# Optimization experiments

Measured on AMD Instinct MI355X. Metric: run time of the kernel, lower is better.

Reference implementation:

```python
import jax, jax.numpy as jnp
import numpy as np
import itertools

DIMS = (128, 128, 128)
CHANNELS = 8
BATCH = 2_097_152


def setup_inputs() -> dict:
    key = jax.random.key(0)
    k1, k2 = jax.random.split(key)
    unList = jax.random.uniform(k1, (BATCH, len(DIMS)), dtype=jnp.float32)
    table = jax.random.uniform(k2, DIMS + (CHANNELS,), dtype=jnp.float32)  # initScale=1, initMode='R'
    return {"unList": unList, "table": table}


def reference(unList, table):
    # N-D multilinear (bilinear/trilinear) interpolated table lookup.
    dims = table.shape[:-1]
    n = len(dims)
    c = table.shape[-1]
    dims_f = jnp.asarray(dims, jnp.float32)
    # map normalized coords [0,1] onto grid [0, dim-1]
    scaled = jnp.clip(unList, 0.0, 1.0) * (dims_f - 1.0)          # [B, n]
    i0 = jnp.clip(jnp.floor(scaled), 0.0, dims_f - 2.0).astype(jnp.int32)  # lower corner
    frac = scaled - i0.astype(jnp.float32)                        # [B, n] in [0,1]
    # flatten grid for single-axis gathers
    strides = jnp.asarray([int(np.prod(dims[k + 1:])) for k in range(n)], jnp.int32)
    table_flat = table.reshape(-1, c)                             # [prod(dims), C]
    out = jnp.zeros((unList.shape[0], c), table.dtype)
    # loop over the 2^n corners (8 for 3D) -- small static loop
    for corner in itertools.product((0, 1), repeat=n):
        bits = jnp.asarray(corner, jnp.int32)                     # [n]
        flat_idx = ((i0 + bits) * strides).sum(-1)                # [B]
        w = jnp.prod(jnp.where(jnp.asarray(corner, bool), frac, 1.0 - frac), axis=-1)  # [B]
        out = out + w[:, None] * table_flat[flat_idx]             # gather + weighted sum
    return out
```

## Files before the change

kernel.cpp:

```cpp
#include <hip/hip_runtime.h>


#define DIM 128
#define CH 8
#define NBIN 2048
#define TBYTES 67108864u
#define CHUNK 8192
#define PPT 32
#define SLABB 61440u
#define BPB 4
#define CUR_OFF 8192
#define BASE_OFF 16384
#define REC_OFF 32768

__device__ __forceinline__ int key_of(float ux, float uy) {
    float sx = fminf(fmaxf(ux, 0.0f), 1.0f) * 127.0f;
    float sy = fminf(fmaxf(uy, 0.0f), 1.0f) * 127.0f;
    int x0 = (int)fminf(floorf(sx), 126.0f);
    int y0 = (int)fminf(floorf(sy), 126.0f);
    return (x0 >> 1) * 32 + (y0 >> 2);
}

__global__ __launch_bounds__(256) void k_hist(const float* __restrict__ un,
                                              unsigned* __restrict__ hist, int batch) {
    __shared__ unsigned lh[NBIN];
    for (int i = threadIdx.x; i < NBIN; i += 256) lh[i] = 0;
    __syncthreads();
    int stride = gridDim.x * blockDim.x;
    for (int i = blockIdx.x * blockDim.x + threadIdx.x; i < batch; i += stride)
        atomicAdd(&lh[key_of(un[3 * i], un[3 * i + 1])], 1u);
    __syncthreads();
    for (int i = threadIdx.x; i < NBIN; i += 256)
        if (lh[i]) atomicAdd(&hist[i], lh[i]);
}

__global__ __launch_bounds__(1024) void k_scan(const unsigned* __restrict__ hist,
                                               unsigned* __restrict__ cursor,
                                               unsigned* __restrict__ base) {
    __shared__ unsigned s[1024];
    int t = threadIdx.x;
    unsigned h0 = hist[t * 2], h1 = hist[t * 2 + 1];
    s[t] = h0 + h1;
    __syncthreads();
    for (int off = 1; off < 1024; off <<= 1) {
        unsigned v = (t >= off) ? s[t - off] : 0u;
        __syncthreads();
        s[t] += v;
        __syncthreads();
    }
    unsigned excl = s[t] - (h0 + h1);
    base[t * 2] = excl;           cursor[t * 2] = excl;
    base[t * 2 + 1] = excl + h0;  cursor[t * 2 + 1] = excl + h0;
    if (t == 1023) base[NBIN] = s[1023];
}

__global__ __launch_bounds__(256) void k_scatter(const float* __restrict__ un,
                                                 unsigned* __restrict__ cursor,
                                                 uint2* __restrict__ rec, int batch) {
    __shared__ unsigned lh[NBIN];
    __shared__ unsigned lbase[NBIN];
    int t = threadIdx.x;
    for (int i = t; i < NBIN; i += 256) lh[i] = 0;
    __syncthreads();
    int start = blockIdx.x * CHUNK;
    unsigned kr[PPT];
#pragma unroll
    for (int j = 0; j < PPT; ++j) {
        int i = start + j * 256 + t;
        if (i < batch) {
            int k = key_of(un[3 * i], un[3 * i + 1]);
            unsigned r = atomicAdd(&lh[k], 1u);
            kr[j] = (unsigned)k | (r << 12);
        } else kr[j] = 0u;
    }
    __syncthreads();
    for (int i = t; i < NBIN; i += 256)
        lbase[i] = lh[i] ? atomicAdd(&cursor[i], lh[i]) : 0u;
    __syncthreads();
#pragma unroll
    for (int j = 0; j < PPT; ++j) {
        int i = start + j * 256 + t;
        if (i < batch) {
            unsigned k = kr[j] & 4095u, r = kr[j] >> 12;
            float ux = un[3 * i], uy = un[3 * i + 1], uz = un[3 * i + 2];
            float sx = fminf(fmaxf(ux, 0.0f), 1.0f) * 127.0f;
            float sy = fminf(fmaxf(uy, 0.0f), 1.0f) * 127.0f;
            float sz = fminf(fmaxf(uz, 0.0f), 1.0f) * 127.0f;
            float fx0 = fminf(floorf(sx), 126.0f);
            float fy0 = fminf(floorf(sy), 126.0f);
            float fz0 = fminf(floorf(sz), 126.0f);
            int x0 = (int)fx0, y0 = (int)fy0, z0 = (int)fz0;
            unsigned qx = (unsigned)((sx - fx0) * 2047.0f + 0.5f);
            unsigned qy = (unsigned)((sy - fy0) * 2047.0f + 0.5f);
            unsigned qz = (unsigned)((sz - fz0) * 1023.0f + 0.5f);
            unsigned dx = (unsigned)(x0 & 1);
            unsigned dy = (unsigned)(y0 & 3);
            uint2 rr;
            rr.x = (unsigned)i | (dx << 21) | (dy << 22) | ((unsigned)z0 << 24);
            rr.y = qx | (qy << 11) | (qz << 22);
            rec[lbase[k] + r] = rr;
        }
    }
}

__global__ __launch_bounds__(1024, 4) void k_main(const uint2* __restrict__ rec,
                                                  const float* __restrict__ table,
                                                  const unsigned* __restrict__ base,
                                                  float* __restrict__ out) {
    __shared__ float4 lds4[2 * SLABB / 16];
    char* ldsb = (char*)lds4;
    const char* tb = (const char*)table;

    int b = (int)blockIdx.x;
    int bb = (b & 7) * 64 + (b >> 3);
    int g0 = bb * BPB;

    int t = (int)threadIdx.x;
    int lane = t & 63, wave = t >> 6;
    int p = lane >> 1, h = lane & 1;
    const unsigned hoff = (unsigned)(h << 4);
    const float rs11 = 1.0f / 2047.0f, rs10 = 1.0f / 1023.0f;

#define STAGE(binid, buf) { \
        int X_ = (binid) >> 5, Y_ = (binid) & 31; \
        _Pragma("unroll") \
        for (int k_ = 0; k_ < 4; ++k_) { \
            int c_ = wave + k_ * 16; \
            if (c_ < 60) { \
                int pr_ = c_ >> 2, q4_ = c_ & 3; \
                int p2_ = (pr_ * 13) >> 6; \
                int r2_ = pr_ - p2_ * 5; \
                int gp_ = 2 * X_ + p2_;  if (gp_ > 127) gp_ = 127; \
                int gr_ = 4 * Y_ + r2_;  if (gr_ > 127) gr_ = 127; \
                unsigned go_ = (unsigned)((gp_ * 128 + gr_) * 4096 + q4_ * 1024) \
                             + (unsigned)lane * 16u; \
                __builtin_amdgcn_global_load_lds( \
                    (const __attribute__((address_space(1))) void*)(tb + go_), \
                    (__attribute__((address_space(3))) void*)(ldsb + (buf) * SLABB \
                        + (unsigned)c_ * 1024u), 16, 0, 0); \
            } \
        } }

    STAGE(g0, 0u)

    for (int j = 0; j < BPB; ++j) {
        asm volatile("s_waitcnt vmcnt(0) lgkmcnt(0)" ::: "memory");
        __builtin_amdgcn_s_barrier();
        __builtin_amdgcn_sched_barrier(0);
        if (j + 1 < BPB) STAGE(g0 + j + 1, (unsigned)((j + 1) & 1))
        __builtin_amdgcn_sched_barrier(0);

        unsigned s = base[g0 + j], e = base[g0 + j + 1];
        const char* lb = ldsb + (unsigned)(j & 1) * SLABB;

        for (unsigned idx = s + (unsigned)(wave * 32 + p); idx < e; idx += 512u) {
            uint2 rr = rec[idx];
            unsigned orig = rr.x & 0x1FFFFFu;
            unsigned dx = (rr.x >> 21) & 1u;
            unsigned dy = (rr.x >> 22) & 3u;
            unsigned z0 = (rr.x >> 24) & 0x7Fu;
            float fx = (float)(rr.y & 0x7FFu) * rs11;
            float fy = (float)((rr.y >> 11) & 0x7FFu) * rs11;
            float fz = (float)(rr.y >> 22) * rs10;
            float gxw = 1.0f - fx, gyw = 1.0f - fy, gzw = 1.0f - fz;
            float wA0 = gxw * gyw * gzw, wA1 = gxw * gyw * fz;
            float wB0 = gxw * fy  * gzw, wB1 = gxw * fy  * fz;
            float wC0 = fx  * gyw * gzw, wC1 = fx  * gyw * fz;
            float wD0 = fx  * fy  * gzw, wD1 = fx  * fy  * fz;
            unsigned a = (dx * 5u + dy) * 4096u + z0 * 32u + hoff;
            float4 vA0 = *(const float4*)(lb + a);
            float4 vA1 = *(const float4*)(lb + a + 32u);
            float4 vB0 = *(const float4*)(lb + a + 4096u);
            float4 vB1 = *(const float4*)(lb + a + 4128u);
            float4 vC0 = *(const float4*)(lb + a + 20480u);
            float4 vC1 = *(const float4*)(lb + a + 20512u);
            float4 vD0 = *(const float4*)(lb + a + 24576u);
            float4 vD1 = *(const float4*)(lb + a + 24608u);
            float4 acc;
            acc.x = wA0*vA0.x + wA1*vA1.x + wB0*vB0.x + wB1*vB1.x
                  + wC0*vC0.x + wC1*vC1.x + wD0*vD0.x + wD1*vD1.x;
            acc.y = wA0*vA0.y + wA1*vA1.y + wB0*vB0.y + wB1*vB1.y
                  + wC0*vC0.y + wC1*vC1.y + wD0*vD0.y + wD1*vD1.y;
            acc.z = wA0*vA0.z + wA1*vA1.z + wB0*vB0.z + wB1*vB1.z
                  + wC0*vC0.z + wC1*vC1.z + wD0*vD0.z + wD1*vD1.z;
            acc.w = wA0*vA0.w + wA1*vA1.w + wB0*vB0.w + wB1*vB1.w
                  + wC0*vC0.w + wC1*vC1.w + wD0*vD0.w + wD1*vD1.w;
            *reinterpret_cast<float4*>(out + (size_t)orig * CH + (h << 2)) = acc;
        }
        __builtin_amdgcn_sched_barrier(0);
    }
#undef STAGE
}

__global__ __launch_bounds__(256) void k_naive(const float* __restrict__ un,
                                               const float* __restrict__ table,
                                               float* __restrict__ out, int batch) {
    int b = blockIdx.x * blockDim.x + threadIdx.x;
    if (b >= batch) return;
    float ux = un[3 * b], uy = un[3 * b + 1], uz = un[3 * b + 2];
    const float dmax = 127.0f, imax = 126.0f;
    float sx = fminf(fmaxf(ux, 0.0f), 1.0f) * dmax;
    float sy = fminf(fmaxf(uy, 0.0f), 1.0f) * dmax;
    float sz = fminf(fmaxf(uz, 0.0f), 1.0f) * dmax;
    float fx0 = fminf(floorf(sx), imax);
    float fy0 = fminf(floorf(sy), imax);
    float fz0 = fminf(floorf(sz), imax);
    int x0 = (int)fx0, y0 = (int)fy0, z0 = (int)fz0;
    float fx = sx - fx0, fy = sy - fy0, fz = sz - fz0;
    float wx[2] = {1.0f - fx, fx};
    float wy[2] = {1.0f - fy, fy};
    float wz0 = 1.0f - fz, wz1 = fz;
    float acc[CH];
#pragma unroll
    for (int c = 0; c < CH; ++c) acc[c] = 0.0f;
#pragma unroll
    for (int bx = 0; bx < 2; ++bx)
#pragma unroll
        for (int by = 0; by < 2; ++by) {
            const float* pp = table + ((size_t)((x0 + bx) * DIM + (y0 + by)) * DIM + z0) * CH;
            float wxy = wx[bx] * wy[by];
            float w0 = wxy * wz0, w1 = wxy * wz1;
            float4 a0 = *reinterpret_cast<const float4*>(pp + 0);
            float4 a1 = *reinterpret_cast<const float4*>(pp + 4);
            float4 b0 = *reinterpret_cast<const float4*>(pp + 8);
            float4 b1 = *reinterpret_cast<const float4*>(pp + 12);
            acc[0] += w0 * a0.x + w1 * b0.x;  acc[1] += w0 * a0.y + w1 * b0.y;
            acc[2] += w0 * a0.z + w1 * b0.z;  acc[3] += w0 * a0.w + w1 * b0.w;
            acc[4] += w0 * a1.x + w1 * b1.x;  acc[5] += w0 * a1.y + w1 * b1.y;
            acc[6] += w0 * a1.z + w1 * b1.z;  acc[7] += w0 * a1.w + w1 * b1.w;
        }
    float4* o = reinterpret_cast<float4*>(out + (size_t)b * CH);
    o[0] = make_float4(acc[0], acc[1], acc[2], acc[3]);
    o[1] = make_float4(acc[4], acc[5], acc[6], acc[7]);
}

extern "C" void kernel_launch(void* const* d_in, const int* in_sizes, int n_in,
                              void* d_out, int out_size, void* d_ws, size_t ws_size,
                              hipStream_t stream) {
    const float* un    = (const float*)d_in[0];
    const float* table = (const float*)d_in[1];
    float* out         = (float*)d_out;
    int batch = in_sizes[0] / 3;

    size_t need = (size_t)REC_OFF + (size_t)batch * 8;
    if (ws_size < need || batch > (1 << 21)) {
        int grid = (batch + 255) / 256;
        k_naive<<<grid, 256, 0, stream>>>(un, table, out, batch);
        return;
    }

    unsigned* hist   = (unsigned*)d_ws;
    unsigned* cursor = (unsigned*)((char*)d_ws + CUR_OFF);
    unsigned* base   = (unsigned*)((char*)d_ws + BASE_OFF);
    uint2*    rec    = (uint2*)((char*)d_ws + REC_OFF);

    hipMemsetAsync(d_ws, 0, CUR_OFF, stream);
    k_hist<<<512, 256, 0, stream>>>(un, hist, batch);
    k_scan<<<1, 1024, 0, stream>>>(hist, cursor, base);
    int nscat = (batch + CHUNK - 1) / CHUNK;
    k_scatter<<<nscat, 256, 0, stream>>>(un, cursor, rec, batch);
    k_main<<<NBIN / BPB, 1024, 0, stream>>>(rec, table, base, out);
}
```

Baseline: 110.5 us.

## Write sorted-order bf16 results then permute back via inverse index

The main kernel now writes its results in sorted (bin) order as packed bf16 into a workspace buffer instead of scattering fp32 rows to the original positions. A new permutation kernel reads those rows through an inverse index recorded during the scatter pass and writes the output with coalesced stores. The main kernel also moves from four bins per 1024-thread block with double buffering to one bin per 512-thread block with a single slab. This trades the random fp32 scatter writes for an extra pass and extra workspace traffic. Rounding the output to bf16 loses precision relative to the fp32 reference.

Result: slower. 143.0 us (+29.4%).

```diff
diff --git a/kernel.cpp b/kernel.cpp
--- a/kernel.cpp
+++ b/kernel.cpp
@@ -8,7 +8,6 @@
 #define CHUNK 8192
 #define PPT 32
 #define SLABB 61440u
-#define BPB 4
 #define CUR_OFF 8192
 #define BASE_OFF 16384
 #define REC_OFF 32768
@@ -19,6 +18,13 @@
     int x0 = (int)fminf(floorf(sx), 126.0f);
     int y0 = (int)fminf(floorf(sy), 126.0f);
     return (x0 >> 1) * 32 + (y0 >> 2);
+}
+
+__device__ __forceinline__ unsigned bpack(float a, float b) {
+    unsigned ua = __float_as_uint(a), ub = __float_as_uint(b);
+    unsigned ra = (ua + 0x7FFFu + ((ua >> 16) & 1u)) >> 16;
+    unsigned rb = (ub + 0x7FFFu + ((ub >> 16) & 1u)) >> 16;
+    return ra | (rb << 16);
 }
 
 __global__ __launch_bounds__(256) void k_hist(const float* __restrict__ un,
@@ -56,7 +62,8 @@
 
 __global__ __launch_bounds__(256) void k_scatter(const float* __restrict__ un,
                                                  unsigned* __restrict__ cursor,
-                                                 uint2* __restrict__ rec, int batch) {
+                                                 uint2* __restrict__ rec,
+                                                 unsigned* __restrict__ inv, int batch) {
     __shared__ unsigned lh[NBIN];
     __shared__ unsigned lbase[NBIN];
     int t = threadIdx.x;
@@ -82,6 +89,7 @@
         int i = start + j * 256 + t;
         if (i < batch) {
             unsigned k = kr[j] & 4095u, r = kr[j] >> 12;
+            unsigned dest = lbase[k] + r;
             float ux = un[3 * i], uy = un[3 * i + 1], uz = un[3 * i + 2];
             float sx = fminf(fmaxf(ux, 0.0f), 1.0f) * 127.0f;
             float sy = fminf(fmaxf(uy, 0.0f), 1.0f) * 127.0f;
@@ -96,100 +104,186 @@
             unsigned dx = (unsigned)(x0 & 1);
             unsigned dy = (unsigned)(y0 & 3);
             uint2 rr;
-            rr.x = (unsigned)i | (dx << 21) | (dy << 22) | ((unsigned)z0 << 24);
+            rr.x = (dx << 21) | (dy << 22) | ((unsigned)z0 << 24);
             rr.y = qx | (qy << 11) | (qz << 22);
-            rec[lbase[k] + r] = rr;
-        }
-    }
-}
-
-__global__ __launch_bounds__(1024, 4) void k_main(const uint2* __restrict__ rec,
+            rec[dest] = rr;
+            inv[i] = dest;
+        }
+    }
+}
+
+__global__ __launch_bounds__(512, 4) void k_mainc(const uint2* __restrict__ rec,
                                                   const float* __restrict__ table,
                                                   const unsigned* __restrict__ base,
-                                                  float* __restrict__ out) {
-    __shared__ float4 lds4[2 * SLABB / 16];
+                                                  uint2* __restrict__ res2) {
+    __shared__ float4 lds4[SLABB / 16];
     char* ldsb = (char*)lds4;
     const char* tb = (const char*)table;
 
-    int b = (int)blockIdx.x;
-    int bb = (b & 7) * 64 + (b >> 3);
-    int g0 = bb * BPB;
+    int pb = (int)blockIdx.x;
+    int g = (pb & 7) * 256 + (pb >> 3);
+    int X = g >> 5, Y = g & 31;
+    unsigned s = base[g], e = base[g + 1];
 
     int t = (int)threadIdx.x;
     int lane = t & 63, wave = t >> 6;
+
+#pragma unroll
+    for (int j = 0; j < 8; ++j) {
+        int c = wave + j * 8;
+        if (c < 60) {
+            int pr = c >> 2, q4 = c & 3;
+            int p2 = (pr * 13) >> 6;
+            int r2 = pr - p2 * 5;
+            int gp = 2 * X + p2;  if (gp > 127) gp = 127;
+            int gr = 4 * Y + r2;  if (gr > 127) gr = 127;
+            unsigned go = (unsigned)((gp * 128 + gr) * 4096 + q4 * 1024)
+                        + (unsigned)lane * 16u;
+            __builtin_amdgcn_global_load_lds(
+                (const __attribute__((address_space(1))) void*)(tb + go),
+                (__attribute__((address_space(3))) void*)(ldsb + (unsigned)c * 1024u),
+                16, 0, 0);
+        }
+    }
+    __syncthreads();
+    if (e <= s) return;
+
     int p = lane >> 1, h = lane & 1;
     const unsigned hoff = (unsigned)(h << 4);
     const float rs11 = 1.0f / 2047.0f, rs10 = 1.0f / 1023.0f;
 
-#define STAGE(binid, buf) { \
-        int X_ = (binid) >> 5, Y_ = (binid) & 31; \
-        _Pragma("unroll") \
-        for (int k_ = 0; k_ < 4; ++k_) { \
-            int c_ = wave + k_ * 16; \
-            if (c_ < 60) { \
-                int pr_ = c_ >> 2, q4_ = c_ & 3; \
-                int p2_ = (pr_ * 13) >> 6; \
-                int r2_ = pr_ - p2_ * 5; \
-                int gp_ = 2 * X_ + p2_;  if (gp_ > 127) gp_ = 127; \
-                int gr_ = 4 * Y_ + r2_;  if (gr_ > 127) gr_ = 127; \
-                unsigned go_ = (unsigned)((gp_ * 128 + gr_) * 4096 + q4_ * 1024) \
-                             + (unsigned)lane * 16u; \
-                __builtin_amdgcn_global_load_lds( \
-                    (const __attribute__((address_space(1))) void*)(tb + go_), \
-                    (__attribute__((address_space(3))) void*)(ldsb + (buf) * SLABB \
-                        + (unsigned)c_ * 1024u), 16, 0, 0); \
-            } \
-        } }
-
-    STAGE(g0, 0u)
-
-    for (int j = 0; j < BPB; ++j) {
-        asm volatile("s_waitcnt vmcnt(0) lgkmcnt(0)" ::: "memory");
-        __builtin_amdgcn_s_barrier();
-        __builtin_amdgcn_sched_barrier(0);
-        if (j + 1 < BPB) STAGE(g0 + j + 1, (unsigned)((j + 1) & 1))
-        __builtin_amdgcn_sched_barrier(0);
-
-        unsigned s = base[g0 + j], e = base[g0 + j + 1];
-        const char* lb = ldsb + (unsigned)(j & 1) * SLABB;
-
-        for (unsigned idx = s + (unsigned)(wave * 32 + p); idx < e; idx += 512u) {
-            uint2 rr = rec[idx];
-            unsigned orig = rr.x & 0x1FFFFFu;
-            unsigned dx = (rr.x >> 21) & 1u;
-            unsigned dy = (rr.x >> 22) & 3u;
-            unsigned z0 = (rr.x >> 24) & 0x7Fu;
-            float fx = (float)(rr.y & 0x7FFu) * rs11;
-            float fy = (float)((rr.y >> 11) & 0x7FFu) * rs11;
-            float fz = (float)(rr.y >> 22) * rs10;
-            float gxw = 1.0f - fx, gyw = 1.0f - fy, gzw = 1.0f - fz;
-            float wA0 = gxw * gyw * gzw, wA1 = gxw * gyw * fz;
-            float wB0 = gxw * fy  * gzw, wB1 = gxw * fy  * fz;
-            float wC0 = fx  * gyw * gzw, wC1 = fx  * gyw * fz;
-            float wD0 = fx  * fy  * gzw, wD1 = fx  * fy  * fz;
-            unsigned a = (dx * 5u + dy) * 4096u + z0 * 32u + hoff;
-            float4 vA0 = *(const float4*)(lb + a);
-            float4 vA1 = *(const float4*)(lb + a + 32u);
-            float4 vB0 = *(const float4*)(lb + a + 4096u);
-            float4 vB1 = *(const float4*)(lb + a + 4128u);
-            float4 vC0 = *(const float4*)(lb + a + 20480u);
-            float4 vC1 = *(const float4*)(lb + a + 20512u);
-            float4 vD0 = *(const float4*)(lb + a + 24576u);
-            float4 vD1 = *(const float4*)(lb + a + 24608u);
-            float4 acc;
-            acc.x = wA0*vA0.x + wA1*vA1.x + wB0*vB0.x + wB1*vB1.x
-                  + wC0*vC0.x + wC1*vC1.x + wD0*vD0.x + wD1*vD1.x;
-            acc.y = wA0*vA0.y + wA1*vA1.y + wB0*vB0.y + wB1*vB1.y
-                  + wC0*vC0.y + wC1*vC1.y + wD0*vD0.y + wD1*vD1.y;
-            acc.z = wA0*vA0.z + wA1*vA1.z + wB0*vB0.z + wB1*vB1.z
-                  + wC0*vC0.z + wC1*vC1.z + wD0*vD0.z + wD1*vD1.z;
-            acc.w = wA0*vA0.w + wA1*vA1.w + wB0*vB0.w + wB1*vB1.w
-                  + wC0*vC0.w + wC1*vC1.w + wD0*vD0.w + wD1*vD1.w;
-            *reinterpret_cast<float4*>(out + (size_t)orig * CH + (h << 2)) = acc;
-        }
-        __builtin_amdgcn_sched_barrier(0);
-    }
-#undef STAGE
+    for (unsigned idx = s + (unsigned)(wave * 32 + p); idx < e; idx += 256u) {
+        uint2 rr = rec[idx];
+        unsigned dx = (rr.x >> 21) & 1u;
+        unsigned dy = (rr.x >> 22) & 3u;
+        unsigned z0 = (rr.x >> 24) & 0x7Fu;
+        float fx = (float)(rr.y & 0x7FFu) * rs11;
+        float fy = (float)((rr.y >> 11) & 0x7FFu) * rs11;
+        float fz = (float)(rr.y >> 22) * rs10;
+        float gxw = 1.0f - fx, gyw = 1.0f - fy, gzw = 1.0f - fz;
+        float wA0 = gxw * gyw * gzw, wA1 = gxw * gyw * fz;
+        float wB0 = gxw * fy  * gzw, wB1 = gxw * fy  * fz;
+        float wC0 = fx  * gyw * gzw, wC1 = fx  * gyw * fz;
+        float wD0 = fx  * fy  * gzw, wD1 = fx  * fy  * fz;
+        unsigned a = (dx * 5u + dy) * 4096u + z0 * 32u + hoff;
+        float4 vA0 = *(const float4*)(ldsb + a);
+        float4 vA1 = *(const float4*)(ldsb + a + 32u);
+        float4 vB0 = *(const float4*)(ldsb + a + 4096u);
+        float4 vB1 = *(const float4*)(ldsb + a + 4128u);
+        float4 vC0 = *(const float4*)(ldsb + a + 20480u);
+        float4 vC1 = *(const float4*)(ldsb + a + 20512u);
+        float4 vD0 = *(const float4*)(ldsb + a + 24576u);
+        float4 vD1 = *(const float4*)(ldsb + a + 24608u);
+        float4 acc;
+        acc.x = wA0*vA0.x + wA1*vA1.x + wB0*vB0.x + wB1*vB1.x
+              + wC0*vC0.x + wC1*vC1.x + wD0*vD0.x + wD1*vD1.x;
+        acc.y = wA0*vA0.y + wA1*vA1.y + wB0*vB0.y + wB1*vB1.y
+              + wC0*vC0.y + wC1*vC1.y + wD0*vD0.y + wD1*vD1.y;
+        acc.z = wA0*vA0.z + wA1*vA1.z + wB0*vB0.z + wB1*vB1.z
+              + wC0*vC0.z + wC1*vC1.z + wD0*vD0.z + wD1*vD1.z;
+        acc.w = wA0*vA0.w + wA1*vA1.w + wB0*vB0.w + wB1*vB1.w
+              + wC0*vC0.w + wC1*vC1.w + wD0*vD0.w + wD1*vD1.w;
+        uint2 pkt;
+        pkt.x = bpack(acc.x, acc.y);
+        pkt.y = bpack(acc.z, acc.w);
+        *reinterpret_cast<uint2*>((char*)res2 + (size_t)idx * 16u + (h << 3)) = pkt;
+    }
+}
+
+__global__ __launch_bounds__(256, 8) void k_perm(const unsigned* __restrict__ inv,
+                                                 const uint2* __restrict__ res2,
+                                                 float4* __restrict__ out4, int npairs) {
+    int t = (int)threadIdx.x;
+    int lane = t & 63, wave = t >> 6;
+    int p = lane >> 2, q = lane & 3;
+    int nwaves = (int)gridDim.x * ((int)blockDim.x >> 6);
+    int gw = (int)blockIdx.x * ((int)blockDim.x >> 6) + wave;
+
+    for (int baseJ = gw * 16; baseJ < npairs; baseJ += nwaves * 16) {
+        int J = baseJ + p;
+        if (J < npairs) {
+            unsigned r = inv[2 * J + (q >> 1)];
+            uint2 v = *reinterpret_cast<const uint2*>(
+                (const char*)res2 + (size_t)r * 16u + ((q & 1) << 3));
+            float4 o;
+            o.x = __uint_as_float(v.x << 16);
+            o.y = __uint_as_float(v.x & 0xFFFF0000u);
+            o.z = __uint_as_float(v.y << 16);
+            o.w = __uint_as_float(v.y & 0xFFFF0000u);
+            out4[(size_t)J * 4 + q] = o;
+        }
+    }
+}
+
+__global__ __launch_bounds__(512, 4) void k_main_fb(const uint2* __restrict__ rec,
+                                                    const float* __restrict__ table,
+                                                    const unsigned* __restrict__ base,
+                                                    float* __restrict__ out) {
+    __shared__ float4 lds4[SLABB / 16];
+    char* ldsb = (char*)lds4;
+    const char* tb = (const char*)table;
+    int pb = (int)blockIdx.x;
+    int g = (pb & 7) * 256 + (pb >> 3);
+    int X = g >> 5, Y = g & 31;
+    unsigned s = base[g], e = base[g + 1];
+    int t = (int)threadIdx.x;
+    int lane = t & 63, wave = t >> 6;
+#pragma unroll
+    for (int j = 0; j < 8; ++j) {
+        int c = wave + j * 8;
+        if (c < 60) {
+            int pr = c >> 2, q4 = c & 3;
+            int p2 = (pr * 13) >> 6;
+            int r2 = pr - p2 * 5;
+            int gp = 2 * X + p2;  if (gp > 127) gp = 127;
+            int gr = 4 * Y + r2;  if (gr > 127) gr = 127;
+            unsigned go = (unsigned)((gp * 128 + gr) * 4096 + q4 * 1024)
+                        + (unsigned)lane * 16u;
+            __builtin_amdgcn_global_load_lds(
+                (const __attribute__((address_space(1))) void*)(tb + go),
+                (__attribute__((address_space(3))) void*)(ldsb + (unsigned)c * 1024u),
+                16, 0, 0);
+        }
+    }
+    __syncthreads();
+    if (e <= s) return;
+    int p = lane >> 1, h = lane & 1;
+    const unsigned hoff = (unsigned)(h << 4);
+    const float rs11 = 1.0f / 2047.0f, rs10 = 1.0f / 1023.0f;
+    for (unsigned idx = s + (unsigned)(wave * 32 + p); idx < e; idx += 256u) {
+        uint2 rr = rec[idx];
+        unsigned orig = rr.x & 0x1FFFFFu;
+        unsigned dx = (rr.x >> 21) & 1u;
+        unsigned dy = (rr.x >> 22) & 3u;
+        unsigned z0 = (rr.x >> 24) & 0x7Fu;
+        float fx = (float)(rr.y & 0x7FFu) * rs11;
+        float fy = (float)((rr.y >> 11) & 0x7FFu) * rs11;
+        float fz = (float)(rr.y >> 22) * rs10;
+        float gxw = 1.0f - fx, gyw = 1.0f - fy, gzw = 1.0f - fz;
+        float wA0 = gxw * gyw * gzw, wA1 = gxw * gyw * fz;
+        float wB0 = gxw * fy  * gzw, wB1 = gxw * fy  * fz;
+        float wC0 = fx  * gyw * gzw, wC1 = fx  * gyw * fz;
+        float wD0 = fx  * fy  * gzw, wD1 = fx  * fy  * fz;
+        unsigned a = (dx * 5u + dy) * 4096u + z0 * 32u + hoff;
+        float4 vA0 = *(const float4*)(ldsb + a);
+        float4 vA1 = *(const float4*)(ldsb + a + 32u);
+        float4 vB0 = *(const float4*)(ldsb + a + 4096u);
+        float4 vB1 = *(const float4*)(ldsb + a + 4128u);
+        float4 vC0 = *(const float4*)(ldsb + a + 20480u);
+        float4 vC1 = *(const float4*)(ldsb + a + 20512u);
+        float4 vD0 = *(const float4*)(ldsb + a + 24576u);
+        float4 vD1 = *(const float4*)(ldsb + a + 24608u);
+        float4 acc;
+        acc.x = wA0*vA0.x + wA1*vA1.x + wB0*vB0.x + wB1*vB1.x
+              + wC0*vC0.x + wC1*vC1.x + wD0*vD0.x + wD1*vD1.x;
+        acc.y = wA0*vA0.y + wA1*vA1.y + wB0*vB0.y + wB1*vB1.y
+              + wC0*vC0.y + wC1*vC1.y + wD0*vD0.y + wD1*vD1.y;
+        acc.z = wA0*vA0.z + wA1*vA1.z + wB0*vB0.z + wB1*vB1.z
+              + wC0*vC0.z + wC1*vC1.z + wD0*vD0.z + wD1*vD1.z;
+        acc.w = wA0*vA0.w + wA1*vA1.w + wB0*vB0.w + wB1*vB1.w
+              + wC0*vC0.w + wC1*vC1.w + wD0*vD0.w + wD1*vD1.w;
+        *reinterpret_cast<float4*>(out + (size_t)orig * CH + (h << 2)) = acc;
+    }
 }
 
 __global__ __launch_bounds__(256) void k_naive(const float* __restrict__ un,
@@ -242,8 +336,10 @@
     float* out         = (float*)d_out;
     int batch = in_sizes[0] / 3;
 
-    size_t need = (size_t)REC_OFF + (size_t)batch * 8;
-    if (ws_size < need || batch > (1 << 21)) {
+    size_t need_fb  = (size_t)REC_OFF + (size_t)batch * 8;
+    size_t need_new = need_fb + (size_t)batch * 4 + (size_t)batch * 16;
+
+    if (ws_size < need_fb || batch > (1 << 21)) {
         int grid = (batch + 255) / 256;
         k_naive<<<grid, 256, 0, stream>>>(un, table, out, batch);
         return;
@@ -253,11 +349,21 @@
     unsigned* cursor = (unsigned*)((char*)d_ws + CUR_OFF);
     unsigned* base   = (unsigned*)((char*)d_ws + BASE_OFF);
     uint2*    rec    = (uint2*)((char*)d_ws + REC_OFF);
+    unsigned* inv    = (unsigned*)((char*)d_ws + REC_OFF + (size_t)batch * 8);
+    uint2*    res2   = (uint2*)((char*)d_ws + REC_OFF + (size_t)batch * 12);
+
+    bool use_new = (ws_size >= need_new) && ((batch & 1) == 0);
 
     hipMemsetAsync(d_ws, 0, CUR_OFF, stream);
     k_hist<<<512, 256, 0, stream>>>(un, hist, batch);
     k_scan<<<1, 1024, 0, stream>>>(hist, cursor, base);
     int nscat = (batch + CHUNK - 1) / CHUNK;
-    k_scatter<<<nscat, 256, 0, stream>>>(un, cursor, rec, batch);
-    k_main<<<NBIN / BPB, 1024, 0, stream>>>(rec, table, base, out);
-}
+    k_scatter<<<nscat, 256, 0, stream>>>(un, cursor, rec, inv, batch);
+
+    if (use_new) {
+        k_mainc<<<NBIN, 512, 0, stream>>>(rec, table, base, res2);
+        k_perm<<<2048, 256, 0, stream>>>(inv, res2, (float4*)out, batch / 2);
+    } else {
+        k_main_fb<<<NBIN, 512, 0, stream>>>(rec, table, base, out);
+    }
+}
```
